# Kernel optimization log

Hardware: AMD Instinct MI355X
Metric: run time of the kernel (lower is better)

## Reference

```python
import jax, jax.numpy as jnp
import numpy as np

NUM_EXPERTS = 64
INPUT_SIZE = 2048
NUM_TOKENS = 16384
TOPK = 8
INIT_STD = 0.02


def setup_inputs() -> dict:
    key = jax.random.key(0)
    k1, k2 = jax.random.split(key)
    input = jax.random.normal(k1, (NUM_TOKENS, INPUT_SIZE), dtype=jnp.float32)
    weight = INIT_STD * jax.random.normal(k2, (NUM_EXPERTS, INPUT_SIZE), dtype=jnp.float32)
    return {"input": input, "weight": weight}


def reference(input, weight):
    # gating GEMM: [N, D] x [E, D]^T -> [N, E]
    logits = jnp.einsum('nd,ed->ne', input, weight)
    n, e = logits.shape
    # pre_softmax=False branch: topk on raw logits, then softmax over selected
    top_scores, top_idx = jax.lax.top_k(logits, TOPK)          # [N, K]
    probs = jax.nn.softmax(top_scores.astype(jnp.float32), axis=-1).astype(logits.dtype)
    rows = jnp.arange(n)[:, None]                               # [N, 1]
    routing_probs = jnp.zeros_like(logits).at[rows, top_idx].set(probs)
    routing_map = jnp.zeros((n, e), dtype=jnp.bool_).at[rows, top_idx].set(True)
    return routing_probs, routing_map
```

## Files before the change

kernel.cpp:

```cpp
#include <hip/hip_runtime.h>
#include <cstdint>
#include <cmath>

#define D_DIM 2048
#define E_DIM 64
#define N_TOK 16384
#define K_TOP 8
#define KSTEP 32
#define TSTEPS 16
#define NFRAG 12

typedef __attribute__((ext_vector_type(8))) short bf16x8;
typedef __attribute__((ext_vector_type(4))) float f32x4;
typedef __attribute__((ext_vector_type(4))) unsigned u32x4;

__device__ inline void split3(const f32x4 v0, const f32x4 v1,
                              bf16x8& h, bf16x8& m, bf16x8& l) {
#pragma unroll
  for (int j = 0; j < 8; ++j) {
    const float x = (j < 4) ? v0[j] : v1[j - 4];
    const unsigned u = __builtin_bit_cast(unsigned, x);
    const unsigned rh = (u + 0x7FFFu + ((u >> 16) & 1u)) & 0xFFFF0000u;
    h[j] = (short)(rh >> 16);
    const float r1 = x - __builtin_bit_cast(float, rh);
    const unsigned u1 = __builtin_bit_cast(unsigned, r1);
    const unsigned rm = (u1 + 0x7FFFu + ((u1 >> 16) & 1u)) & 0xFFFF0000u;
    m[j] = (short)(rm >> 16);
    const float r2 = r1 - __builtin_bit_cast(float, rm);
    l[j] = (short)(__builtin_bit_cast(unsigned, r2) >> 16);
  }
}

__global__ void wprep_kernel(const float* __restrict__ W, uint4* __restrict__ WF) {
  const int gid = blockIdx.x * 256 + threadIdx.x;
  const int lane = gid & 63;
  const int et = (gid >> 6) & 3;
  const int ks = gid >> 8;
  const int e = et * 16 + (lane & 15);
  const int kg = lane >> 4;
  const float* src = W + (size_t)e * D_DIM + ks * KSTEP + kg * 8;
  const f32x4 a = *(const f32x4*)src;
  const f32x4 b = *(const f32x4*)(src + 4);
  bf16x8 h, m, l;
  split3(a, b, h, m, l);
  const int fbase = (ks * NFRAG + et * 3) * 64 + lane;
  WF[fbase] = __builtin_bit_cast(uint4, h);
  WF[fbase + 64] = __builtin_bit_cast(uint4, m);
  WF[fbase + 128] = __builtin_bit_cast(uint4, l);
}

#define BCV(x) __builtin_bit_cast(bf16x8, x)
#define MM(d, A, B) d = __builtin_amdgcn_mfma_f32_16x16x32_bf16(A, BCV(B), d, 0, 0, 0)

#define GL4(dst, voff, sbase, IMM)                              \
  asm volatile("global_load_dwordx4 %0, %1, %2 offset:" #IMM    \
               : "=v"(dst) : "v"(voff), "s"(sbase) : "memory")

#define SB0 __builtin_amdgcn_sched_barrier(0)
#define WAITV(N) asm volatile("s_waitcnt vmcnt(" #N ")" ::: "memory")

__global__ __launch_bounds__(64, 2)
void gemm_partial(const float* __restrict__ X, const uint4* __restrict__ WF,
                  float* __restrict__ Part) {
  const int bid = blockIdx.x;
  const int ks = bid & 3;
  const int mt = bid >> 2;
  const int l = threadIdx.x;
  const int col = l & 15;
  const int kg = l >> 4;
  const int tok0 = mt * 32;

  const char* sB = (const char*)WF + (size_t)(ks * TSTEPS) * 12288;
  const char* sX = (const char*)X + (size_t)tok0 * 8192 + (size_t)ks * 2048;

  const unsigned vB0 = (unsigned)(l * 16);
  const unsigned vB1 = vB0 + 4096;
  const unsigned vB2 = vB0 + 8192;
  const unsigned vX0 = (unsigned)(col * 8192 + kg * 32);
  const unsigned vX1 = vX0 + 16 * 8192;

  f32x4 acc0[8], acc1[8];
#pragma unroll
  for (int i = 0; i < 8; ++i) { acc0[i] = (f32x4)0.f; acc1[i] = (f32x4)0.f; }

  u32x4 bE[NFRAG], bO[NFRAG];
  f32x4 xE[4], xO[4];

#define ISSUE_STEP(bS, xS, t)                          \
  do {                                                 \
    const char* sB_ = sB + (size_t)(t) * 12288;        \
    const char* sX_ = sX + (size_t)(t) * 128;          \
    GL4(bS[0], vB0, sB_, 0);                           \
    GL4(bS[1], vB0, sB_, 1024);                        \
    GL4(bS[2], vB0, sB_, 2048);                        \
    GL4(bS[3], vB0, sB_, 3072);                        \
    GL4(bS[4], vB1, sB_, 0);                           \
    GL4(bS[5], vB1, sB_, 1024);                        \
    GL4(bS[6], vB1, sB_, 2048);                        \
    GL4(bS[7], vB1, sB_, 3072);                        \
    GL4(bS[8], vB2, sB_, 0);                           \
    GL4(bS[9], vB2, sB_, 1024);                        \
    GL4(bS[10], vB2, sB_, 2048);                       \
    GL4(bS[11], vB2, sB_, 3072);                       \
    GL4(xS[0], vX0, sX_, 0);                           \
    GL4(xS[1], vX0, sX_, 16);                          \
    GL4(xS[2], vX1, sX_, 0);                           \
    GL4(xS[3], vX1, sX_, 16);                          \
  } while (0)

#define CRUNCH(bS, AH0, AM0, AL0, AH1, AM1, AL1)                                         \
  do {                                                                                   \
    _Pragma("unroll") for (int et = 0; et < 4; ++et) {                                   \
      MM(acc0[et], AH0, bS[et * 3]);     MM(acc0[4 + et], AH1, bS[et * 3]);              \
    }                                                                                    \
    _Pragma("unroll") for (int et = 0; et < 4; ++et) {                                   \
      MM(acc1[et], AH0, bS[et * 3 + 1]); MM(acc1[4 + et], AH1, bS[et * 3 + 1]);          \
    }                                                                                    \
    _Pragma("unroll") for (int et = 0; et < 4; ++et) {                                   \
      MM(acc1[et], AM0, bS[et * 3]);     MM(acc1[4 + et], AM1, bS[et * 3]);              \
    }                                                                                    \
    _Pragma("unroll") for (int et = 0; et < 4; ++et) {                                   \
      MM(acc1[et], AH0, bS[et * 3 + 2]); MM(acc1[4 + et], AH1, bS[et * 3 + 2]);          \
    }                                                                                    \
    _Pragma("unroll") for (int et = 0; et < 4; ++et) {                                   \
      MM(acc1[et], AL0, bS[et * 3]);     MM(acc1[4 + et], AL1, bS[et * 3]);              \
    }                                                                                    \
    _Pragma("unroll") for (int et = 0; et < 4; ++et) {                                   \
      MM(acc1[et], AM0, bS[et * 3 + 1]); MM(acc1[4 + et], AM1, bS[et * 3 + 1]);          \
    }                                                                                    \
  } while (0)

#define PHASE(bS, xS)                                  \
  do {                                                 \
    bf16x8 ah0, am0, al0, ah1, am1, al1;               \
    split3(xS[0], xS[1], ah0, am0, al0);               \
    split3(xS[2], xS[3], ah1, am1, al1);               \
    CRUNCH(bS, ah0, am0, al0, ah1, am1, al1);          \
    SB0;                                               \
  } while (0)

  ISSUE_STEP(bE, xE, 0);
  ISSUE_STEP(bO, xO, 1);
  WAITV(16);
  SB0;

#pragma unroll 1
  for (int t = 0; t < TSTEPS - 2; t += 2) {
    PHASE(bE, xE);
    ISSUE_STEP(bE, xE, t + 2);
    WAITV(16);
    SB0;
    PHASE(bO, xO);
    ISSUE_STEP(bO, xO, t + 3);
    WAITV(16);
    SB0;
  }
  PHASE(bE, xE);
  WAITV(0);
  SB0;
  PHASE(bO, xO);

#pragma unroll
  for (int mt2 = 0; mt2 < 2; ++mt2)
#pragma unroll
    for (int q = 0; q < 4; ++q) {
      const int tok = tok0 + mt2 * 16 + kg * 4 + q;
      float* dst = Part + ((size_t)ks * N_TOK + tok) * E_DIM + col;
#pragma unroll
      for (int et = 0; et < 4; ++et)
        dst[et * 16] = acc0[mt2 * 4 + et][q] + acc1[mt2 * 4 + et][q];
    }
}

__global__ __launch_bounds__(256)
void reduce_router(const float* __restrict__ Part,
                   float* __restrict__ Pout, float* __restrict__ Mout) {
  const int lane = threadIdx.x & 63;
  const int gw = blockIdx.x * 4 + (threadIdx.x >> 6);

#pragma unroll 1
  for (int j = 0; j < 8; ++j) {
    const int tok = gw * 8 + j;
    const size_t base = (size_t)tok * E_DIM + lane;
    float v = Part[base];
    v += Part[(size_t)1 * N_TOK * E_DIM + base];
    v += Part[(size_t)2 * N_TOK * E_DIM + base];
    v += Part[(size_t)3 * N_TOK * E_DIM + base];

    float topv[K_TOP];
    int topi[K_TOP];
#pragma unroll
    for (int kk = 0; kk < K_TOP; ++kk) {
      float m = v;
#pragma unroll
      for (int off = 32; off > 0; off >>= 1)
        m = fmaxf(m, __shfl_xor(m, off, 64));
      const unsigned long long bal = __ballot(v == m);
      const int li = __ffsll(bal) - 1;
      topv[kk] = m;
      topi[kk] = li;
      if (lane == li) v = -INFINITY;
    }

    float p[K_TOP], sum = 0.f;
#pragma unroll
    for (int kk = 0; kk < K_TOP; ++kk) {
      p[kk] = expf(topv[kk] - topv[0]);
      sum += p[kk];
    }
    const float inv = 1.f / sum;

    float pv = 0.f, mv = 0.f;
#pragma unroll
    for (int kk = 0; kk < K_TOP; ++kk)
      if (topi[kk] == lane) { pv = p[kk] * inv; mv = 1.f; }

    Pout[(size_t)tok * E_DIM + lane] = pv;
    Mout[(size_t)tok * E_DIM + lane] = mv;
  }
}

extern "C" void kernel_launch(void* const* d_in, const int* in_sizes, int n_in,
                              void* d_out, int out_size, void* d_ws, size_t ws_size,
                              hipStream_t stream) {
  const float* X = (const float*)d_in[0];
  const float* W = (const float*)d_in[1];
  float* P = (float*)d_out;
  float* M = P + (size_t)N_TOK * E_DIM;

  uint4* WF = (uint4*)d_ws;
  float* Part = (float*)((char*)d_ws + (size_t)(1 << 20));

  wprep_kernel<<<dim3(64), dim3(256), 0, stream>>>(W, WF);
  gemm_partial<<<dim3(2048), dim3(64), 0, stream>>>(X, WF, Part);
  reduce_router<<<dim3(512), dim3(256), 0, stream>>>(Part, P, M);
}
```

Measured before the change: 62.07 us.

## Share weight fragments across four waves via LDS with async global-to-LDS staging

```diff
diff --git a/kernel.cpp b/kernel.cpp
--- a/kernel.cpp
+++ b/kernel.cpp
@@ -12,7 +12,6 @@
 
 typedef __attribute__((ext_vector_type(8))) short bf16x8;
 typedef __attribute__((ext_vector_type(4))) float f32x4;
-typedef __attribute__((ext_vector_type(4))) unsigned u32x4;
 
 __device__ inline void split3(const f32x4 v0, const f32x4 v1,
                               bf16x8& h, bf16x8& m, bf16x8& l) {
@@ -58,117 +57,130 @@
 
 #define SB0 __builtin_amdgcn_sched_barrier(0)
 #define WAITV(N) asm volatile("s_waitcnt vmcnt(" #N ")" ::: "memory")
-
-__global__ __launch_bounds__(64, 2)
+#define FENCE asm volatile("" ::: "memory")
+#define BAR __builtin_amdgcn_s_barrier()
+
+__global__ __launch_bounds__(256, 2)
 void gemm_partial(const float* __restrict__ X, const uint4* __restrict__ WF,
                   float* __restrict__ Part) {
+  __shared__ uint4 ldsB[4][NFRAG][64];
+
   const int bid = blockIdx.x;
   const int ks = bid & 3;
-  const int mt = bid >> 2;
-  const int l = threadIdx.x;
+  const int mtile = bid >> 2;
+  const int tid = threadIdx.x;
+  const int w = tid >> 6;
+  const int l = tid & 63;
   const int col = l & 15;
   const int kg = l >> 4;
-  const int tok0 = mt * 32;
-
-  const char* sB = (const char*)WF + (size_t)(ks * TSTEPS) * 12288;
-  const char* sX = (const char*)X + (size_t)tok0 * 8192 + (size_t)ks * 2048;
-
-  const unsigned vB0 = (unsigned)(l * 16);
-  const unsigned vB1 = vB0 + 4096;
-  const unsigned vB2 = vB0 + 8192;
-  const unsigned vX0 = (unsigned)(col * 8192 + kg * 32);
+  const int tokw = mtile * 128 + w * 32;
+
+  const char* sX = (const char*)X + (size_t)(mtile * 128) * 8192 + (size_t)ks * 2048;
+  const char* wfB = (const char*)WF + (size_t)ks * TSTEPS * 12288;
+
+  const unsigned vX0 = (unsigned)(w * 32 * 8192 + col * 8192 + kg * 32);
   const unsigned vX1 = vX0 + 16 * 8192;
 
   f32x4 acc0[8], acc1[8];
 #pragma unroll
   for (int i = 0; i < 8; ++i) { acc0[i] = (f32x4)0.f; acc1[i] = (f32x4)0.f; }
 
-  u32x4 bE[NFRAG], bO[NFRAG];
   f32x4 xE[4], xO[4];
 
-#define ISSUE_STEP(bS, xS, t)                          \
-  do {                                                 \
-    const char* sB_ = sB + (size_t)(t) * 12288;        \
-    const char* sX_ = sX + (size_t)(t) * 128;          \
-    GL4(bS[0], vB0, sB_, 0);                           \
-    GL4(bS[1], vB0, sB_, 1024);                        \
-    GL4(bS[2], vB0, sB_, 2048);                        \
-    GL4(bS[3], vB0, sB_, 3072);                        \
-    GL4(bS[4], vB1, sB_, 0);                           \
-    GL4(bS[5], vB1, sB_, 1024);                        \
-    GL4(bS[6], vB1, sB_, 2048);                        \
-    GL4(bS[7], vB1, sB_, 3072);                        \
-    GL4(bS[8], vB2, sB_, 0);                           \
-    GL4(bS[9], vB2, sB_, 1024);                        \
-    GL4(bS[10], vB2, sB_, 2048);                       \
-    GL4(bS[11], vB2, sB_, 3072);                       \
-    GL4(xS[0], vX0, sX_, 0);                           \
-    GL4(xS[1], vX0, sX_, 16);                          \
-    GL4(xS[2], vX1, sX_, 0);                           \
-    GL4(xS[3], vX1, sX_, 16);                          \
+#define LOADX(xS, t)                          \
+  do {                                        \
+    const char* sX_ = sX + (size_t)(t) * 128; \
+    GL4(xS[0], vX0, sX_, 0);                  \
+    GL4(xS[1], vX0, sX_, 16);                 \
+    GL4(xS[2], vX1, sX_, 0);                  \
+    GL4(xS[3], vX1, sX_, 16);                 \
   } while (0)
 
-#define CRUNCH(bS, AH0, AM0, AL0, AH1, AM1, AL1)                                         \
-  do {                                                                                   \
-    _Pragma("unroll") for (int et = 0; et < 4; ++et) {                                   \
-      MM(acc0[et], AH0, bS[et * 3]);     MM(acc0[4 + et], AH1, bS[et * 3]);              \
-    }                                                                                    \
-    _Pragma("unroll") for (int et = 0; et < 4; ++et) {                                   \
-      MM(acc1[et], AH0, bS[et * 3 + 1]); MM(acc1[4 + et], AH1, bS[et * 3 + 1]);          \
-    }                                                                                    \
-    _Pragma("unroll") for (int et = 0; et < 4; ++et) {                                   \
-      MM(acc1[et], AM0, bS[et * 3]);     MM(acc1[4 + et], AM1, bS[et * 3]);              \
-    }                                                                                    \
-    _Pragma("unroll") for (int et = 0; et < 4; ++et) {                                   \
-      MM(acc1[et], AH0, bS[et * 3 + 2]); MM(acc1[4 + et], AH1, bS[et * 3 + 2]);          \
-    }                                                                                    \
-    _Pragma("unroll") for (int et = 0; et < 4; ++et) {                                   \
-      MM(acc1[et], AL0, bS[et * 3]);     MM(acc1[4 + et], AL1, bS[et * 3]);              \
-    }                                                                                    \
-    _Pragma("unroll") for (int et = 0; et < 4; ++et) {                                   \
-      MM(acc1[et], AM0, bS[et * 3 + 1]); MM(acc1[4 + et], AM1, bS[et * 3 + 1]);          \
-    }                                                                                    \
+#define STAGE(t, buf)                                                        \
+  do {                                                                       \
+    _Pragma("unroll") for (int c = 0; c < 3; ++c) {                          \
+      const int f_ = w * 3 + c;                                              \
+      const char* g_ = wfB + (size_t)(t) * 12288 + f_ * 1024 + l * 16;       \
+      __builtin_amdgcn_global_load_lds(                                      \
+          (const __attribute__((address_space(1))) void*)g_,                 \
+          (__attribute__((address_space(3))) void*)&ldsB[buf][f_][0], 16, 0, 0); \
+    }                                                                        \
   } while (0)
 
-#define PHASE(bS, xS)                                  \
-  do {                                                 \
-    bf16x8 ah0, am0, al0, ah1, am1, al1;               \
-    split3(xS[0], xS[1], ah0, am0, al0);               \
-    split3(xS[2], xS[3], ah1, am1, al1);               \
-    CRUNCH(bS, ah0, am0, al0, ah1, am1, al1);          \
-    SB0;                                               \
+#define CRUNCH(buf, xS)                                                      \
+  do {                                                                       \
+    bf16x8 ah0, am0, al0, ah1, am1, al1;                                     \
+    split3(xS[0], xS[1], ah0, am0, al0);                                     \
+    split3(xS[2], xS[3], ah1, am1, al1);                                     \
+    const uint4* fb_ = &ldsB[buf][0][0];                                     \
+    uint4 f0 = fb_[0 * 64 + l], f1 = fb_[1 * 64 + l], f2 = fb_[2 * 64 + l];  \
+    uint4 f3 = fb_[3 * 64 + l], f4 = fb_[4 * 64 + l], f5 = fb_[5 * 64 + l];  \
+    uint4 f6 = fb_[6 * 64 + l], f7 = fb_[7 * 64 + l], f8 = fb_[8 * 64 + l];  \
+    uint4 f9 = fb_[9 * 64 + l], f10 = fb_[10 * 64 + l], f11 = fb_[11 * 64 + l]; \
+    MM(acc0[0], ah0, f0); MM(acc0[4], ah1, f0);                              \
+    MM(acc0[1], ah0, f3); MM(acc0[5], ah1, f3);                              \
+    MM(acc0[2], ah0, f6); MM(acc0[6], ah1, f6);                              \
+    MM(acc0[3], ah0, f9); MM(acc0[7], ah1, f9);                              \
+    MM(acc1[0], ah0, f1); MM(acc1[4], ah1, f1);                              \
+    MM(acc1[1], ah0, f4); MM(acc1[5], ah1, f4);                              \
+    MM(acc1[2], ah0, f7); MM(acc1[6], ah1, f7);                              \
+    MM(acc1[3], ah0, f10); MM(acc1[7], ah1, f10);                            \
+    MM(acc1[0], am0, f0); MM(acc1[4], am1, f0);                              \
+    MM(acc1[1], am0, f3); MM(acc1[5], am1, f3);                              \
+    MM(acc1[2], am0, f6); MM(acc1[6], am1, f6);                              \
+    MM(acc1[3], am0, f9); MM(acc1[7], am1, f9);                              \
+    MM(acc1[0], ah0, f2); MM(acc1[4], ah1, f2);                              \
+    MM(acc1[1], ah0, f5); MM(acc1[5], ah1, f5);                              \
+    MM(acc1[2], ah0, f8); MM(acc1[6], ah1, f8);                              \
+    MM(acc1[3], ah0, f11); MM(acc1[7], ah1, f11);                            \
+    MM(acc1[0], al0, f0); MM(acc1[4], al1, f0);                              \
+    MM(acc1[1], al0, f3); MM(acc1[5], al1, f3);                              \
+    MM(acc1[2], al0, f6); MM(acc1[6], al1, f6);                              \
+    MM(acc1[3], al0, f9); MM(acc1[7], al1, f9);                              \
+    MM(acc1[0], am0, f1); MM(acc1[4], am1, f1);                              \
+    MM(acc1[1], am0, f4); MM(acc1[5], am1, f4);                              \
+    MM(acc1[2], am0, f7); MM(acc1[6], am1, f7);                              \
+    MM(acc1[3], am0, f10); MM(acc1[7], am1, f10);                            \
   } while (0)
 
-  ISSUE_STEP(bE, xE, 0);
-  ISSUE_STEP(bO, xO, 1);
-  WAITV(16);
-  SB0;
+  STAGE(0, 0);
+  STAGE(1, 1);
+  LOADX(xE, 0);
+  LOADX(xO, 1);
 
 #pragma unroll 1
   for (int t = 0; t < TSTEPS - 2; t += 2) {
-    PHASE(bE, xE);
-    ISSUE_STEP(bE, xE, t + 2);
-    WAITV(16);
+    STAGE(t + 2, (t + 2) & 3);
+    WAITV(7);
     SB0;
-    PHASE(bO, xO);
-    ISSUE_STEP(bO, xO, t + 3);
-    WAITV(16);
+    FENCE; BAR; FENCE;
+    CRUNCH(t & 3, xE);
+    LOADX(xE, t + 2);
+    STAGE(t + 3, (t + 3) & 3);
+    WAITV(7);
     SB0;
+    FENCE; BAR; FENCE;
+    CRUNCH((t + 1) & 3, xO);
+    LOADX(xO, t + 3);
   }
-  PHASE(bE, xE);
+  WAITV(4);
+  SB0;
+  FENCE; BAR; FENCE;
+  CRUNCH(2, xE);
   WAITV(0);
   SB0;
-  PHASE(bO, xO);
-
-#pragma unroll
-  for (int mt2 = 0; mt2 < 2; ++mt2)
+  FENCE; BAR; FENCE;
+  CRUNCH(3, xO);
+
+#pragma unroll
+  for (int half = 0; half < 2; ++half)
 #pragma unroll
     for (int q = 0; q < 4; ++q) {
-      const int tok = tok0 + mt2 * 16 + kg * 4 + q;
+      const int tok = tokw + half * 16 + kg * 4 + q;
       float* dst = Part + ((size_t)ks * N_TOK + tok) * E_DIM + col;
 #pragma unroll
       for (int et = 0; et < 4; ++et)
-        dst[et * 16] = acc0[mt2 * 4 + et][q] + acc1[mt2 * 4 + et][q];
+        dst[et * 16] = acc0[half * 4 + et][q] + acc1[half * 4 + et][q];
     }
 }
 
@@ -232,6 +244,6 @@
   float* Part = (float*)((char*)d_ws + (size_t)(1 << 20));
 
   wprep_kernel<<<dim3(64), dim3(256), 0, stream>>>(W, WF);
-  gemm_partial<<<dim3(2048), dim3(64), 0, stream>>>(X, WF, Part);
+  gemm_partial<<<dim3(512), dim3(256), 0, stream>>>(X, WF, Part);
   reduce_router<<<dim3(512), dim3(256), 0, stream>>>(Part, P, M);
 }
```

New measurement: 59.20 us. -4.6%, faster.
